# Kernel tuning notes

Measured on AMD Instinct MI355X. Metric: run time of the kernel, lower is better.

## Reference

```python
import jax, jax.numpy as jnp
import numpy as np

T, B, D_IN, D_H = 512, 64, 1024, 1024
SIGMA = 0.01


def setup_inputs() -> dict:
    key = jax.random.key(0)
    ks = jax.random.split(key, 7)
    X = jax.random.normal(ks[0], (T, B, D_IN), dtype=jnp.float32)
    state = jnp.zeros((B, D_H), dtype=jnp.float32)
    W_xr = jax.random.normal(ks[1], (D_IN, D_H), dtype=jnp.float32) * SIGMA
    W_hr = jax.random.normal(ks[2], (D_H, D_H), dtype=jnp.float32) * SIGMA
    b_r = jnp.zeros((D_H,), dtype=jnp.float32)
    W_xz = jax.random.normal(ks[3], (D_IN, D_H), dtype=jnp.float32) * SIGMA
    W_hz = jax.random.normal(ks[4], (D_H, D_H), dtype=jnp.float32) * SIGMA
    b_z = jnp.zeros((D_H,), dtype=jnp.float32)
    W_xh = jax.random.normal(ks[5], (D_IN, D_H), dtype=jnp.float32) * SIGMA
    W_hh = jax.random.normal(ks[6], (D_H, D_H), dtype=jnp.float32) * SIGMA
    b_h = jnp.zeros((D_H,), dtype=jnp.float32)
    return {"X": X, "state": state,
            "W_xr": W_xr, "W_hr": W_hr, "b_r": b_r,
            "W_xz": W_xz, "W_hz": W_hz, "b_z": b_z,
            "W_xh": W_xh, "W_hh": W_hh, "b_h": b_h}


def reference(X, state, W_xr, W_hr, b_r, W_xz, W_hz, b_z, W_xh, W_hh, b_h):
    # Precompute all input projections in one big batched matmul each
    # (the sequential dependency is only through the hidden state).
    Xr = jnp.einsum('tbi,ih->tbh', X, W_xr) + b_r  # [T, B, H]
    Xz = jnp.einsum('tbi,ih->tbh', X, W_xz) + b_z
    Xh = jnp.einsum('tbi,ih->tbh', X, W_xh) + b_h

    def step(h, inputs):
        xr, xz, xh = inputs
        R = jax.nn.sigmoid(xr + h @ W_hr)
        Z = jax.nn.sigmoid(xz + h @ W_hz)
        H_hat = jnp.tanh(xh + (R * h) @ W_hh)
        h_new = Z * h + (1.0 - Z) * H_hat
        return h_new, h_new

    final_state, outputs = jax.lax.scan(step, state, (Xr, Xz, Xh))
    return outputs, final_state
```

## Files before the change

kernel.cpp:

```cpp
#include <hip/hip_runtime.h>
#include <cmath>

typedef unsigned short u16;
typedef unsigned long long u64;
typedef __attribute__((ext_vector_type(4))) float f32x4;
typedef __attribute__((ext_vector_type(8))) __bf16 bf16x8;
typedef unsigned short u16x4 __attribute__((ext_vector_type(4)));
typedef unsigned short u16x8 __attribute__((ext_vector_type(8)));

#define T_STEPS 512
#define NBLK 64
#define FINAL_OFF 33554432u

#define OFF_XR   0ull
#define OFF_XZ   (OFF_XR + 67108864ull)
#define OFF_XH   (OFF_XZ + 67108864ull)
#define OFF_WXRT (OFF_XH + 67108864ull)
#define OFF_WXZT (OFF_WXRT + 2097152ull)
#define OFF_WXHT (OFF_WXZT + 2097152ull)
#define OFF_WHRT (OFF_WXHT + 2097152ull)
#define OFF_WHZT (OFF_WHRT + 2097152ull)
#define OFF_WHHT (OFF_WHZT + 2097152ull)
#define OFF_HBF  (OFF_WHHT + 2097152ull)
#define OFF_RHBF (OFF_HBF + 131072ull)
#define OFF_HF32 (OFF_RHBF + 131072ull)
#define OFF_BAR  (OFF_HF32 + 262144ull)
#define BAR_BYTES 65600ull

__device__ __forceinline__ u16 f2bf(float f) {
    unsigned u = __builtin_bit_cast(unsigned, f);
    unsigned r = (u + 0x7FFFu + ((u >> 16) & 1u)) >> 16;
    return (u16)r;
}
__device__ __forceinline__ float bf2f(u16 h) {
    unsigned u = ((unsigned)h) << 16;
    return __builtin_bit_cast(float, u);
}
#define MFMA16 __builtin_amdgcn_mfma_f32_16x16x32_bf16

__device__ __forceinline__ void sta16(u16* p, u16 v) {
    __hip_atomic_store(p, v, __ATOMIC_RELAXED, __HIP_MEMORY_SCOPE_AGENT);
}
__device__ __forceinline__ void sta32(unsigned* p, unsigned v) {
    __hip_atomic_store(p, v, __ATOMIC_RELAXED, __HIP_MEMORY_SCOPE_AGENT);
}
__device__ __forceinline__ unsigned lda32(const unsigned* p) {
    return __hip_atomic_load(p, __ATOMIC_RELAXED, __HIP_MEMORY_SCOPE_AGENT);
}

#define LD_A4(dst, vo, base)                                          \
    asm volatile("global_load_dwordx4 %0, %1, %2 sc0 sc1"             \
                 : "=v"(dst) : "v"(vo), "s"(base))

#define FLAG_STRIDE 32u

__global__ __launch_bounds__(256) void transpose_cvt(
    const float* __restrict__ W0, const float* __restrict__ W1, const float* __restrict__ W2,
    const float* __restrict__ W3, const float* __restrict__ W4, const float* __restrict__ W5,
    u16* __restrict__ D0, u16* __restrict__ D1, u16* __restrict__ D2,
    u16* __restrict__ D3, u16* __restrict__ D4, u16* __restrict__ D5)
{
    const float* S[6] = {W0, W1, W2, W3, W4, W5};
    u16* D[6] = {D0, D1, D2, D3, D4, D5};
    int z = blockIdx.z;
    const float* W = S[z];
    u16* Dt = D[z];
    __shared__ float tile[32][33];
    int bx = blockIdx.x * 32, by = blockIdx.y * 32;
    int tx = threadIdx.x & 31, ty = threadIdx.x >> 5;
    for (int i = ty; i < 32; i += 8)
        tile[i][tx] = W[(size_t)(by + i) * 1024 + bx + tx];
    __syncthreads();
    for (int i = ty; i < 32; i += 8)
        Dt[(size_t)(bx + i) * 1024 + by + tx] = f2bf(tile[tx][i]);
}

__global__ __launch_bounds__(256, 2) void proj_gemm(
    const float* __restrict__ X,
    const u16* __restrict__ Wt0, const u16* __restrict__ Wt1, const u16* __restrict__ Wt2,
    const float* __restrict__ b0, const float* __restrict__ b1, const float* __restrict__ b2,
    u16* __restrict__ P0, u16* __restrict__ P1, u16* __restrict__ P2)
{
    int z = blockIdx.z;
    const u16* Wt = (z == 0) ? Wt0 : (z == 1) ? Wt1 : Wt2;
    const float* bias = (z == 0) ? b0 : (z == 1) ? b1 : b2;
    u16* P = (z == 0) ? P0 : (z == 1) ? P1 : P2;

    __shared__ u16 Asm[128][72];
    __shared__ u16 Bsm[128][72];

    int tid = threadIdx.x, lane = tid & 63, w = tid >> 6;
    int m0 = blockIdx.y * 128, n0 = blockIdx.x * 128;
    int mw = (w >> 1) * 64, nw = (w & 1) * 64;
    int l15 = lane & 15, lq = lane >> 4;

    f32x4 zero = {0.f, 0.f, 0.f, 0.f};
    f32x4 acc[4][4];
    #pragma unroll
    for (int mi = 0; mi < 4; ++mi)
        #pragma unroll
        for (int nj = 0; nj < 4; ++nj) acc[mi][nj] = zero;

    for (int k0 = 0; k0 < 1024; k0 += 64) {
        #pragma unroll
        for (int i = 0; i < 8; ++i) {
            int flat = i * 256 + tid;
            int r = flat >> 4, c4 = flat & 15;
            float4 v = *(const float4*)(X + (size_t)(m0 + r) * 1024 + k0 + c4 * 4);
            u16x4 pk = {f2bf(v.x), f2bf(v.y), f2bf(v.z), f2bf(v.w)};
            *(u16x4*)&Asm[r][c4 * 4] = pk;
        }
        #pragma unroll
        for (int i = 0; i < 4; ++i) {
            int flat = i * 256 + tid;
            int n = flat >> 3, seg = flat & 7;
            *(u16x8*)&Bsm[n][seg * 8] = *(const u16x8*)(Wt + (size_t)(n0 + n) * 1024 + k0 + seg * 8);
        }
        __syncthreads();
        #pragma unroll
        for (int kk = 0; kk < 2; ++kk) {
            bf16x8 af[4], bg[4];
            #pragma unroll
            for (int mi = 0; mi < 4; ++mi)
                af[mi] = *(const bf16x8*)&Asm[mw + mi * 16 + l15][kk * 32 + lq * 8];
            #pragma unroll
            for (int nj = 0; nj < 4; ++nj)
                bg[nj] = *(const bf16x8*)&Bsm[nw + nj * 16 + l15][kk * 32 + lq * 8];
            #pragma unroll
            for (int mi = 0; mi < 4; ++mi)
                #pragma unroll
                for (int nj = 0; nj < 4; ++nj)
                    acc[mi][nj] = MFMA16(af[mi], bg[nj], acc[mi][nj], 0, 0, 0);
        }
        __syncthreads();
    }
    #pragma unroll
    for (int mi = 0; mi < 4; ++mi)
        #pragma unroll
        for (int nj = 0; nj < 4; ++nj)
            #pragma unroll
            for (int r = 0; r < 4; ++r) {
                int m = m0 + mw + mi * 16 + lq * 4 + r;
                int n = n0 + nw + nj * 16 + l15;
                float v = acc[mi][nj][r] + bias[n];
                P[(size_t)m * 1024 + n] = f2bf(v);
            }
}

__global__ __launch_bounds__(256, 1) void gru_rec(
    const u16* __restrict__ XR, const u16* __restrict__ XZ, const u16* __restrict__ XH,
    const u16* __restrict__ Whrt, const u16* __restrict__ Whzt, const u16* __restrict__ Whht,
    const float* __restrict__ state,
    u16* __restrict__ hbf, u16* __restrict__ rhbf,
    unsigned* __restrict__ bar, float* __restrict__ out)
{
    __shared__ u16 Wsm[48 * 1024];

    const int b = blockIdx.x, tid = threadIdx.x;
    const int lane = tid & 63, mi = tid >> 6;
    const int n15 = lane & 15, q = lane >> 4;
    const int k7 = n15 & 7;
    const int colg = 16 * b + n15;
    const int rot = (((b >> 1) + ((b & 1) << 4)) + mi * 8) & 31;
    const u64 own_bit = 1ull << b;

    {
        int r0 = tid >> 3, seg = tid & 7;
        #pragma unroll
        for (int pass = 0; pass < 2; ++pass) {
            int row = pass * 32 + r0;
            if (row < 48) {
                const u16* src = (row < 16) ? (Whrt + (size_t)(16 * b + row) * 1024)
                               : (row < 32) ? (Whzt + (size_t)(16 * b + row - 16) * 1024)
                                            : (Whht + (size_t)(16 * b + row - 32) * 1024);
                #pragma unroll
                for (int v = 0; v < 16; ++v) {
                    int chunk = seg * 16 + v;
                    int phys = chunk ^ (row & 7);
                    *(u16x8*)&Wsm[row * 1024 + phys * 8] = *(const u16x8*)(src + chunk * 8);
                }
            }
        }
    }
    const unsigned tbase = (unsigned)((mi * 64 + b) * 256);
    f32x4 hcar;
    #pragma unroll
    for (int r = 0; r < 4; ++r) {
        int row = mi * 16 + q * 4 + r;
        float v = state[row * 1024 + colg];
        hcar[r] = v;
        sta16(hbf + tbase + (q * 4 + r) * 16 + n15, f2bf(v));
    }
    asm volatile("s_waitcnt vmcnt(0)" ::: "memory");
    if (lane == 0) sta32(bar + (unsigned)((b << 2) | mi) * FLAG_STRIDE, 1u);
    __syncthreads();

    const u64 hb64 = (u64)hbf;
    const u64 rb64 = (u64)rhbf;
    const unsigned vbA = (unsigned)(mi * 32768 + (q >> 1) * 512 + n15 * 32 + (q & 1) * 16);
    const unsigned* fp = bar + (unsigned)((lane << 2) | mi) * FLAG_STRIDE;
    unsigned* myflag = bar + (unsigned)((b << 2) | mi) * FLAG_STRIDE;

    for (int t = 0; t < T_STEPS; ++t) {
        f32x4 zreg;
        {
            u16 xr16[4], xz16[4];
            #pragma unroll
            for (int r = 0; r < 4; ++r) {
                size_t xoff = (size_t)t * 65536 + (mi * 16 + q * 4 + r) * 1024 + colg;
                xr16[r] = XR[xoff];
                xz16[r] = XZ[xoff];
            }
            f32x4 a[32];
            const unsigned T1 = 2u * t + 1u;
            u64 rdy = __ballot(lda32(fp) >= T1) | own_bit;
            #pragma unroll
            for (int i = 0; i < 32; ++i) {
                int kb = (i + rot) & 31;
                u64 need = 3ull << (2 * kb);
                while ((rdy & need) != need) {
                    __builtin_amdgcn_s_sleep(1);
                    rdy = __ballot(lda32(fp) >= T1) | own_bit;
                }
                LD_A4(a[i], vbA + kb * 1024, hb64);
            }
            asm volatile("s_waitcnt vmcnt(0)" ::: "memory");
            __builtin_amdgcn_sched_barrier(0);

            f32x4 aRa = {0,0,0,0}, aRb = {0,0,0,0}, aZa = {0,0,0,0}, aZb = {0,0,0,0};
            #pragma unroll
            for (int i = 0; i < 32; ++i) {
                int kb = (i + rot) & 31;
                bf16x8 av = __builtin_bit_cast(bf16x8, a[i]);
                int ph = ((kb * 4 + q) ^ k7) * 8;
                bf16x8 br = *(const bf16x8*)&Wsm[n15 * 1024 + ph];
                bf16x8 bz = *(const bf16x8*)&Wsm[(16 + n15) * 1024 + ph];
                if (i & 1) { aRb = MFMA16(av, br, aRb, 0, 0, 0); aZb = MFMA16(av, bz, aZb, 0, 0, 0); }
                else       { aRa = MFMA16(av, br, aRa, 0, 0, 0); aZa = MFMA16(av, bz, aZa, 0, 0, 0); }
            }
            f32x4 accR = aRa + aRb, accZ = aZa + aZb;
            #pragma unroll
            for (int r = 0; r < 4; ++r) {
                float rpre = accR[r] + bf2f(xr16[r]);
                float zpre = accZ[r] + bf2f(xz16[r]);
                float R = 1.f / (1.f + __expf(-rpre));
                zreg[r] = 1.f / (1.f + __expf(-zpre));
                sta16(rhbf + tbase + (q * 4 + r) * 16 + n15, f2bf(R * hcar[r]));
            }
            asm volatile("s_waitcnt vmcnt(0)" ::: "memory");
            if (lane == 0) sta32(myflag, 2u * t + 2u);
        }
        {
            u16 xh16[4];
            #pragma unroll
            for (int r = 0; r < 4; ++r) {
                size_t xoff = (size_t)t * 65536 + (mi * 16 + q * 4 + r) * 1024 + colg;
                xh16[r] = XH[xoff];
            }
            f32x4 a[32];
            const unsigned T2 = 2u * t + 2u;
            u64 rdy = __ballot(lda32(fp) >= T2) | own_bit;
            #pragma unroll
            for (int i = 0; i < 32; ++i) {
                int kb = (i + rot) & 31;
                u64 need = 3ull << (2 * kb);
                while ((rdy & need) != need) {
                    __builtin_amdgcn_s_sleep(1);
                    rdy = __ballot(lda32(fp) >= T2) | own_bit;
                }
                LD_A4(a[i], vbA + kb * 1024, rb64);
            }
            asm volatile("s_waitcnt vmcnt(0)" ::: "memory");
            __builtin_amdgcn_sched_barrier(0);

            f32x4 ca = {0,0,0,0}, cb = {0,0,0,0};
            #pragma unroll
            for (int i = 0; i < 32; ++i) {
                int kb = (i + rot) & 31;
                bf16x8 av = __builtin_bit_cast(bf16x8, a[i]);
                int ph = ((kb * 4 + q) ^ k7) * 8;
                bf16x8 bh = *(const bf16x8*)&Wsm[(32 + n15) * 1024 + ph];
                if (i & 1) cb = MFMA16(av, bh, cb, 0, 0, 0);
                else       ca = MFMA16(av, bh, ca, 0, 0, 0);
            }
            f32x4 acc = ca + cb;
            float hn4[4];
            #pragma unroll
            for (int r = 0; r < 4; ++r) {
                float pre = acc[r] + bf2f(xh16[r]);
                float ax = fabsf(pre);
                float e = __expf(-2.f * ax);
                float th = (1.f - e) / (1.f + e);
                float hh = (pre < 0.f) ? -th : th;
                float hn = zreg[r] * hcar[r] + (1.f - zreg[r]) * hh;
                hn4[r] = hn;
                hcar[r] = hn;
                sta16(hbf + tbase + (q * 4 + r) * 16 + n15, f2bf(hn));
            }
            if (t != T_STEPS - 1) {
                asm volatile("s_waitcnt vmcnt(0)" ::: "memory");
                if (lane == 0) sta32(myflag, 2u * t + 3u);
            }
            #pragma unroll
            for (int r = 0; r < 4; ++r) {
                int idx = (mi * 16 + q * 4 + r) * 1024 + colg;
                size_t xoff = (size_t)t * 65536 + idx;
                out[xoff] = hn4[r];
                if (t == T_STEPS - 1) out[FINAL_OFF + idx] = hn4[r];
            }
        }
    }
}

extern "C" void kernel_launch(void* const* d_in, const int* in_sizes, int n_in,
                              void* d_out, int out_size, void* d_ws, size_t ws_size,
                              hipStream_t stream) {
    (void)in_sizes; (void)n_in; (void)out_size; (void)ws_size;
    const float* X     = (const float*)d_in[0];
    const float* state = (const float*)d_in[1];
    const float* Wxr   = (const float*)d_in[2];
    const float* Whr   = (const float*)d_in[3];
    const float* br    = (const float*)d_in[4];
    const float* Wxz   = (const float*)d_in[5];
    const float* Whz   = (const float*)d_in[6];
    const float* bz    = (const float*)d_in[7];
    const float* Wxh   = (const float*)d_in[8];
    const float* Whh   = (const float*)d_in[9];
    const float* bh    = (const float*)d_in[10];
    float* out = (float*)d_out;
    char* ws = (char*)d_ws;

    u16* XR   = (u16*)(ws + OFF_XR);
    u16* XZ   = (u16*)(ws + OFF_XZ);
    u16* XH   = (u16*)(ws + OFF_XH);
    u16* WXRT = (u16*)(ws + OFF_WXRT);
    u16* WXZT = (u16*)(ws + OFF_WXZT);
    u16* WXHT = (u16*)(ws + OFF_WXHT);
    u16* WHRT = (u16*)(ws + OFF_WHRT);
    u16* WHZT = (u16*)(ws + OFF_WHZT);
    u16* WHHT = (u16*)(ws + OFF_WHHT);
    u16* HBF  = (u16*)(ws + OFF_HBF);
    u16* RHBF = (u16*)(ws + OFF_RHBF);
    unsigned* BAR = (unsigned*)(ws + OFF_BAR);

    hipMemsetAsync(BAR, 0, BAR_BYTES, stream);

    transpose_cvt<<<dim3(32, 32, 6), 256, 0, stream>>>(
        Wxr, Wxz, Wxh, Whr, Whz, Whh,
        WXRT, WXZT, WXHT, WHRT, WHZT, WHHT);

    proj_gemm<<<dim3(8, 256, 3), 256, 0, stream>>>(
        X, WXRT, WXZT, WXHT, br, bz, bh, XR, XZ, XH);

    gru_rec<<<dim3(NBLK), 256, 0, stream>>>(
        XR, XZ, XH, WHRT, WHZT, WHHT, state,
        HBF, RHBF, BAR, out);
}
```

Before: 5.777 ms.

## Halve recurrent grid to 32 blocks with 32 hidden columns each

Runs the persistent GRU recurrence on 32 workgroups instead of 64. Each block now owns 32 hidden columns, so it does twice the MFMA work per step but waits on half as many cross-block flags. W_hr and W_hz stay in a 64-row LDS tile. W_hh no longer fits in LDS and is read straight from global memory (L2) every step, which adds per-step latency on the candidate-state matmul in exchange for cheaper grid-wide synchronisation.

```diff
diff --git a/kernel.cpp b/kernel.cpp
--- a/kernel.cpp
+++ b/kernel.cpp
@@ -9,7 +9,7 @@
 typedef unsigned short u16x8 __attribute__((ext_vector_type(8)));
 
 #define T_STEPS 512
-#define NBLK 64
+#define NBLK2 32
 #define FINAL_OFF 33554432u
 
 #define OFF_XR   0ull
@@ -154,14 +154,13 @@
     u16* __restrict__ hbf, u16* __restrict__ rhbf,
     unsigned* __restrict__ bar, float* __restrict__ out)
 {
-    __shared__ u16 Wsm[48 * 1024];
+    __shared__ u16 Wsm[64 * 1024];
 
     const int b = blockIdx.x, tid = threadIdx.x;
     const int lane = tid & 63, mi = tid >> 6;
     const int n15 = lane & 15, q = lane >> 4;
     const int k7 = n15 & 7;
-    const int colg = 16 * b + n15;
-    const int rot = (((b >> 1) + ((b & 1) << 4)) + mi * 8) & 31;
+    const int rot = (b + mi * 8) & 31;
     const u64 own_bit = 1ull << b;
 
     {
@@ -169,56 +168,61 @@
         #pragma unroll
         for (int pass = 0; pass < 2; ++pass) {
             int row = pass * 32 + r0;
-            if (row < 48) {
-                const u16* src = (row < 16) ? (Whrt + (size_t)(16 * b + row) * 1024)
-                               : (row < 32) ? (Whzt + (size_t)(16 * b + row - 16) * 1024)
-                                            : (Whht + (size_t)(16 * b + row - 32) * 1024);
-                #pragma unroll
-                for (int v = 0; v < 16; ++v) {
-                    int chunk = seg * 16 + v;
-                    int phys = chunk ^ (row & 7);
-                    *(u16x8*)&Wsm[row * 1024 + phys * 8] = *(const u16x8*)(src + chunk * 8);
-                }
+            const u16* src = (row < 32) ? (Whrt + (size_t)(32 * b + row) * 1024)
+                                        : (Whzt + (size_t)(32 * b + row - 32) * 1024);
+            #pragma unroll
+            for (int v = 0; v < 16; ++v) {
+                int chunk = seg * 16 + v;
+                int phys = chunk ^ (row & 7);
+                *(u16x8*)&Wsm[row * 1024 + phys * 8] = *(const u16x8*)(src + chunk * 8);
             }
         }
     }
-    const unsigned tbase = (unsigned)((mi * 64 + b) * 256);
-    f32x4 hcar;
+    const unsigned tbase = (unsigned)((mi * 32 + b) * 512);
+    f32x4 hcar[2];
     #pragma unroll
-    for (int r = 0; r < 4; ++r) {
-        int row = mi * 16 + q * 4 + r;
-        float v = state[row * 1024 + colg];
-        hcar[r] = v;
-        sta16(hbf + tbase + (q * 4 + r) * 16 + n15, f2bf(v));
-    }
+    for (int c = 0; c < 2; ++c)
+        #pragma unroll
+        for (int r = 0; r < 4; ++r) {
+            int row = mi * 16 + q * 4 + r;
+            int col = 32 * b + c * 16 + n15;
+            float v = state[row * 1024 + col];
+            hcar[c][r] = v;
+            sta16(hbf + tbase + (q * 4 + r) * 32 + c * 16 + n15, f2bf(v));
+        }
     asm volatile("s_waitcnt vmcnt(0)" ::: "memory");
     if (lane == 0) sta32(bar + (unsigned)((b << 2) | mi) * FLAG_STRIDE, 1u);
     __syncthreads();
 
     const u64 hb64 = (u64)hbf;
     const u64 rb64 = (u64)rhbf;
-    const unsigned vbA = (unsigned)(mi * 32768 + (q >> 1) * 512 + n15 * 32 + (q & 1) * 16);
+    const unsigned vbA = (unsigned)(mi * 32768 + n15 * 64 + q * 16);
+    const u16* bp0 = Whht + (size_t)(32 * b + n15) * 1024 + q * 8;
+    const u16* bp1 = Whht + (size_t)(32 * b + 16 + n15) * 1024 + q * 8;
     const unsigned* fp = bar + (unsigned)((lane << 2) | mi) * FLAG_STRIDE;
     unsigned* myflag = bar + (unsigned)((b << 2) | mi) * FLAG_STRIDE;
 
     for (int t = 0; t < T_STEPS; ++t) {
-        f32x4 zreg;
+        f32x4 zreg[2];
         {
-            u16 xr16[4], xz16[4];
-            #pragma unroll
-            for (int r = 0; r < 4; ++r) {
-                size_t xoff = (size_t)t * 65536 + (mi * 16 + q * 4 + r) * 1024 + colg;
-                xr16[r] = XR[xoff];
-                xz16[r] = XZ[xoff];
-            }
+            u16 xr16[2][4], xz16[2][4];
+            #pragma unroll
+            for (int c = 0; c < 2; ++c)
+                #pragma unroll
+                for (int r = 0; r < 4; ++r) {
+                    size_t xoff = (size_t)t * 65536 + (mi * 16 + q * 4 + r) * 1024
+                                + 32 * b + c * 16 + n15;
+                    xr16[c][r] = XR[xoff];
+                    xz16[c][r] = XZ[xoff];
+                }
             f32x4 a[32];
             const unsigned T1 = 2u * t + 1u;
             u64 rdy = __ballot(lda32(fp) >= T1) | own_bit;
             #pragma unroll
             for (int i = 0; i < 32; ++i) {
                 int kb = (i + rot) & 31;
-                u64 need = 3ull << (2 * kb);
-                while ((rdy & need) != need) {
+                u64 need = 1ull << kb;
+                while (!(rdy & need)) {
                     __builtin_amdgcn_s_sleep(1);
                     rdy = __ballot(lda32(fp) >= T1) | own_bit;
                 }
@@ -227,44 +231,56 @@
             asm volatile("s_waitcnt vmcnt(0)" ::: "memory");
             __builtin_amdgcn_sched_barrier(0);
 
-            f32x4 aRa = {0,0,0,0}, aRb = {0,0,0,0}, aZa = {0,0,0,0}, aZb = {0,0,0,0};
+            f32x4 aR0 = {0,0,0,0}, aR1 = {0,0,0,0}, aZ0 = {0,0,0,0}, aZ1 = {0,0,0,0};
             #pragma unroll
             for (int i = 0; i < 32; ++i) {
                 int kb = (i + rot) & 31;
                 bf16x8 av = __builtin_bit_cast(bf16x8, a[i]);
                 int ph = ((kb * 4 + q) ^ k7) * 8;
-                bf16x8 br = *(const bf16x8*)&Wsm[n15 * 1024 + ph];
-                bf16x8 bz = *(const bf16x8*)&Wsm[(16 + n15) * 1024 + ph];
-                if (i & 1) { aRb = MFMA16(av, br, aRb, 0, 0, 0); aZb = MFMA16(av, bz, aZb, 0, 0, 0); }
-                else       { aRa = MFMA16(av, br, aRa, 0, 0, 0); aZa = MFMA16(av, bz, aZa, 0, 0, 0); }
-            }
-            f32x4 accR = aRa + aRb, accZ = aZa + aZb;
-            #pragma unroll
-            for (int r = 0; r < 4; ++r) {
-                float rpre = accR[r] + bf2f(xr16[r]);
-                float zpre = accZ[r] + bf2f(xz16[r]);
-                float R = 1.f / (1.f + __expf(-rpre));
-                zreg[r] = 1.f / (1.f + __expf(-zpre));
-                sta16(rhbf + tbase + (q * 4 + r) * 16 + n15, f2bf(R * hcar[r]));
+                bf16x8 br0 = *(const bf16x8*)&Wsm[n15 * 1024 + ph];
+                bf16x8 br1 = *(const bf16x8*)&Wsm[(16 + n15) * 1024 + ph];
+                bf16x8 bz0 = *(const bf16x8*)&Wsm[(32 + n15) * 1024 + ph];
+                bf16x8 bz1 = *(const bf16x8*)&Wsm[(48 + n15) * 1024 + ph];
+                aR0 = MFMA16(av, br0, aR0, 0, 0, 0);
+                aR1 = MFMA16(av, br1, aR1, 0, 0, 0);
+                aZ0 = MFMA16(av, bz0, aZ0, 0, 0, 0);
+                aZ1 = MFMA16(av, bz1, aZ1, 0, 0, 0);
+            }
+            #pragma unroll
+            for (int c = 0; c < 2; ++c) {
+                f32x4 accR = c ? aR1 : aR0;
+                f32x4 accZ = c ? aZ1 : aZ0;
+                #pragma unroll
+                for (int r = 0; r < 4; ++r) {
+                    float rpre = accR[r] + bf2f(xr16[c][r]);
+                    float zpre = accZ[r] + bf2f(xz16[c][r]);
+                    float R = 1.f / (1.f + __expf(-rpre));
+                    zreg[c][r] = 1.f / (1.f + __expf(-zpre));
+                    sta16(rhbf + tbase + (q * 4 + r) * 32 + c * 16 + n15,
+                          f2bf(R * hcar[c][r]));
+                }
             }
             asm volatile("s_waitcnt vmcnt(0)" ::: "memory");
             if (lane == 0) sta32(myflag, 2u * t + 2u);
         }
         {
-            u16 xh16[4];
-            #pragma unroll
-            for (int r = 0; r < 4; ++r) {
-                size_t xoff = (size_t)t * 65536 + (mi * 16 + q * 4 + r) * 1024 + colg;
-                xh16[r] = XH[xoff];
-            }
+            u16 xh16[2][4];
+            #pragma unroll
+            for (int c = 0; c < 2; ++c)
+                #pragma unroll
+                for (int r = 0; r < 4; ++r) {
+                    size_t xoff = (size_t)t * 65536 + (mi * 16 + q * 4 + r) * 1024
+                                + 32 * b + c * 16 + n15;
+                    xh16[c][r] = XH[xoff];
+                }
             f32x4 a[32];
             const unsigned T2 = 2u * t + 2u;
             u64 rdy = __ballot(lda32(fp) >= T2) | own_bit;
             #pragma unroll
             for (int i = 0; i < 32; ++i) {
                 int kb = (i + rot) & 31;
-                u64 need = 3ull << (2 * kb);
-                while ((rdy & need) != need) {
+                u64 need = 1ull << kb;
+                while (!(rdy & need)) {
                     __builtin_amdgcn_s_sleep(1);
                     rdy = __ballot(lda32(fp) >= T2) | own_bit;
                 }
@@ -273,41 +289,47 @@
             asm volatile("s_waitcnt vmcnt(0)" ::: "memory");
             __builtin_amdgcn_sched_barrier(0);
 
-            f32x4 ca = {0,0,0,0}, cb = {0,0,0,0};
+            f32x4 c0a = {0,0,0,0}, c0b = {0,0,0,0}, c1a = {0,0,0,0}, c1b = {0,0,0,0};
             #pragma unroll
             for (int i = 0; i < 32; ++i) {
                 int kb = (i + rot) & 31;
                 bf16x8 av = __builtin_bit_cast(bf16x8, a[i]);
-                int ph = ((kb * 4 + q) ^ k7) * 8;
-                bf16x8 bh = *(const bf16x8*)&Wsm[(32 + n15) * 1024 + ph];
-                if (i & 1) cb = MFMA16(av, bh, cb, 0, 0, 0);
-                else       ca = MFMA16(av, bh, ca, 0, 0, 0);
-            }
-            f32x4 acc = ca + cb;
-            float hn4[4];
-            #pragma unroll
-            for (int r = 0; r < 4; ++r) {
-                float pre = acc[r] + bf2f(xh16[r]);
-                float ax = fabsf(pre);
-                float e = __expf(-2.f * ax);
-                float th = (1.f - e) / (1.f + e);
-                float hh = (pre < 0.f) ? -th : th;
-                float hn = zreg[r] * hcar[r] + (1.f - zreg[r]) * hh;
-                hn4[r] = hn;
-                hcar[r] = hn;
-                sta16(hbf + tbase + (q * 4 + r) * 16 + n15, f2bf(hn));
-            }
+                bf16x8 b0 = *(const bf16x8*)(bp0 + kb * 32);
+                bf16x8 b1 = *(const bf16x8*)(bp1 + kb * 32);
+                if (i & 1) { c0b = MFMA16(av, b0, c0b, 0, 0, 0); c1b = MFMA16(av, b1, c1b, 0, 0, 0); }
+                else       { c0a = MFMA16(av, b0, c0a, 0, 0, 0); c1a = MFMA16(av, b1, c1a, 0, 0, 0); }
+            }
+            f32x4 acc[2];
+            acc[0] = c0a + c0b;
+            acc[1] = c1a + c1b;
+            float hn8[2][4];
+            #pragma unroll
+            for (int c = 0; c < 2; ++c)
+                #pragma unroll
+                for (int r = 0; r < 4; ++r) {
+                    float pre = acc[c][r] + bf2f(xh16[c][r]);
+                    float ax = fabsf(pre);
+                    float e = __expf(-2.f * ax);
+                    float th = (1.f - e) / (1.f + e);
+                    float hh = (pre < 0.f) ? -th : th;
+                    float hn = zreg[c][r] * hcar[c][r] + (1.f - zreg[c][r]) * hh;
+                    hn8[c][r] = hn;
+                    hcar[c][r] = hn;
+                    sta16(hbf + tbase + (q * 4 + r) * 32 + c * 16 + n15, f2bf(hn));
+                }
             if (t != T_STEPS - 1) {
                 asm volatile("s_waitcnt vmcnt(0)" ::: "memory");
                 if (lane == 0) sta32(myflag, 2u * t + 3u);
             }
             #pragma unroll
-            for (int r = 0; r < 4; ++r) {
-                int idx = (mi * 16 + q * 4 + r) * 1024 + colg;
-                size_t xoff = (size_t)t * 65536 + idx;
-                out[xoff] = hn4[r];
-                if (t == T_STEPS - 1) out[FINAL_OFF + idx] = hn4[r];
-            }
+            for (int c = 0; c < 2; ++c)
+                #pragma unroll
+                for (int r = 0; r < 4; ++r) {
+                    int idx = (mi * 16 + q * 4 + r) * 1024 + 32 * b + c * 16 + n15;
+                    size_t xoff = (size_t)t * 65536 + idx;
+                    out[xoff] = hn8[c][r];
+                    if (t == T_STEPS - 1) out[FINAL_OFF + idx] = hn8[c][r];
+                }
         }
     }
 }
@@ -352,7 +374,7 @@
     proj_gemm<<<dim3(8, 256, 3), 256, 0, stream>>>(
         X, WXRT, WXZT, WXHT, br, bz, bh, XR, XZ, XH);
 
-    gru_rec<<<dim3(NBLK), 256, 0, stream>>>(
+    gru_rec<<<dim3(NBLK2), 256, 0, stream>>>(
         XR, XZ, XH, WHRT, WHZT, WHHT, state,
         HBF, RHBF, BAR, out);
 }
```

New measurement: 10.36 ms. +79.3%, slower.
